# Kernel tuning notes

Measured on AMD Instinct MI355X. Metric: run time of the kernel, lower is better.

The kernel has to match this reference:

```python
import jax, jax.numpy as jnp
import numpy as np

B, S, H, F, E, G = 2, 2048, 1024, 2048, 16, 4
EPG = E // G            # experts per group
TOPK = 4                # experts_per_token == gate.top_k
TOPG = min(2, G)        # top groups considered


def setup_inputs() -> dict:
    key = jax.random.key(0)
    ks = jax.random.split(key, 8)
    def w(i, shape, fan):
        return jax.random.normal(ks[i], shape, jnp.float32) / np.sqrt(fan)
    pr = np.ones(E, np.float32)
    pr[::EPG] = 1.2  # expert_priority: first expert of each group boosted
    return dict(
        x=jax.random.normal(ks[0], (B, S, H), jnp.float32),
        Wg=w(1, (H, G), H), bg=jnp.zeros((G,), jnp.float32),
        Wr=w(2, (G, EPG, H), H), br=jnp.zeros((G, EPG), jnp.float32),
        Wc1=w(3, (H, H // 4), H), bc1=jnp.zeros((H // 4,), jnp.float32),
        Wc2=w(4, (H // 4, 1), H // 4), bc2=jnp.zeros((1,), jnp.float32),
        priority=jnp.asarray(pr),
        W1=w(5, (E, H, F), H), b1=jnp.zeros((E, F), jnp.float32),
        W2=w(6, (E, F, H), F), b2=jnp.zeros((E, H), jnp.float32),
    )


def _gate(xf, Wg, bg, Wr, br, Wc1, bc1, Wc2, bc2, priority):
    # xf: [N, H] flattened tokens. Eval mode: no router jitter.
    N = xf.shape[0]
    # confidence estimator: Linear -> GELU -> Linear -> Sigmoid  [N, 1]
    conf = jax.nn.sigmoid(jax.nn.gelu(xf @ Wc1 + bc1, approximate=False) @ Wc2 + bc2)
    group_probs = jax.nn.softmax(xf @ Wg + bg, axis=-1)              # [N, G]
    tg_p, tg_i = jax.lax.top_k(group_probs, TOPG)                    # [N, TOPG]
    # all group routers at once (G*EPG logits per token is tiny)
    logits = (jnp.einsum('nh,geh->nge', xf, Wr) + br) * priority.reshape(G, EPG)[None]
    probs = jax.nn.softmax(logits, axis=-1)                          # [N, G, EPG]
    c = conf[:, :, None]                                             # [N, 1, 1]
    probs = probs * c + (1.0 - c) / EPG                              # confidence blend
    scores = jnp.zeros((N, E), xf.dtype)
    rows = jnp.arange(N)[:, None]
    k_in = min(TOPK, EPG)
    for g in range(TOPG):  # top-group slots are disjoint -> collision-free set
        gid = tg_i[:, g]                                             # [N]
        pg = jnp.take_along_axis(probs, gid[:, None, None], axis=1)[:, 0, :]  # [N, EPG]
        tp, ti = jax.lax.top_k(pg, k_in)                             # [N, k_in]
        glob = ti + gid[:, None] * EPG                               # global expert ids
        scores = scores.at[rows, glob].set(tp * tg_p[:, g:g + 1])
    scores = scores / (scores.sum(-1, keepdims=True) + 1e-9)
    ts, ti2 = jax.lax.top_k(scores, TOPK)
    combine = jnp.zeros_like(scores).at[rows, ti2].set(ts)           # dispatch == combine
    return combine


def reference(x, Wg, bg, Wr, br, Wc1, bc1, Wc2, bc2, priority, W1, b1, W2, b2):
    b, s, h = x.shape
    xf = x.reshape(-1, h)                                            # [N, H]
    combine = _gate(xf, Wg, bg, Wr, br, Wc1, bc1, Wc2, bc2, priority)  # [N, E]
    # Torch loop applies every expert to every token, weighted by combine column.
    hid = jax.nn.gelu(jnp.einsum('nh,ehf->nef', xf, W1) + b1, approximate=False)  # [N,E,F]
    out_e = jnp.einsum('nef,efh->neh', hid, W2) + b2                 # [N, E, H]
    out = jnp.einsum('ne,neh->nh', combine, out_e)                   # [N, H]
    aux_loss = jnp.float32(0.0)  # eval mode
    return out.reshape(b, s, h), aux_loss
```

## Files before the change

### kernel.cpp

```cpp
#include <hip/hip_runtime.h>

#define H_DIM 1024
#define F_DIM 2048
#define NE 16
#define NG 4
#define EPG_C 4
#define NTOK 4096
#define NROWS 16384
#define HID_ROWS (NROWS + 128)
#define TB 8

using bf16x8 = __attribute__((ext_vector_type(8))) short;
using f32x4  = __attribute__((ext_vector_type(4))) float;

__device__ __forceinline__ float gelu_f(float v) {
    return 0.5f * v * (1.0f + erff(v * 0.70710678118654752440f));
}
__device__ __forceinline__ unsigned short f2bf(float f) {
    unsigned int u = __float_as_uint(f);
    u += 0x7FFFu + ((u >> 16) & 1u);
    return (unsigned short)(u >> 16);
}
__device__ __forceinline__ float bf2f(unsigned short s) {
    return __uint_as_float(((unsigned int)s) << 16);
}
__device__ __forceinline__ void split2(float v, unsigned short& hi, unsigned short& lo) {
    hi = f2bf(v);
    lo = f2bf(v - bf2f(hi));
}
__device__ __forceinline__ float wave_red_sum(float v) {
    #pragma unroll
    for (int off = 32; off > 0; off >>= 1) v += __shfl_down(v, off, 64);
    return v;
}
__device__ __forceinline__ void gld16(const void* g, void* l) {
    __builtin_amdgcn_global_load_lds(
        (const __attribute__((address_space(1))) unsigned int*)g,
        (__attribute__((address_space(3))) unsigned int*)l, 16, 0, 0);
}

__global__ __launch_bounds__(256) void zero_kernel(float* __restrict__ out, int n,
                                                   int* __restrict__ counts) {
    int i = blockIdx.x * blockDim.x + threadIdx.x;
    int stride = gridDim.x * blockDim.x;
    for (; i < n; i += stride) out[i] = 0.0f;
    if (blockIdx.x == 0 && threadIdx.x < NE) counts[threadIdx.x] = 0;
}

__global__ __launch_bounds__(256) void splitx_kernel(const float* __restrict__ x,
                                                     unsigned short* __restrict__ xh,
                                                     unsigned short* __restrict__ xl, int n4) {
    int i = blockIdx.x * blockDim.x + threadIdx.x;
    int stride = gridDim.x * blockDim.x;
    for (; i < n4; i += stride) {
        float4 v = ((const float4*)x)[i];
        ushort4 h, l;
        split2(v.x, h.x, l.x); split2(v.y, h.y, l.y);
        split2(v.z, h.z, l.z); split2(v.w, h.w, l.w);
        ((ushort4*)xh)[i] = h;
        ((ushort4*)xl)[i] = l;
    }
}

__global__ __launch_bounds__(256) void splitT_kernel(const float* __restrict__ W,
                                                     unsigned short* __restrict__ Th,
                                                     unsigned short* __restrict__ Tl,
                                                     int K, int N) {
    __shared__ float st[64][65];
    int e = blockIdx.z, kt = blockIdx.y, ntile = blockIdx.x;
    const float* src = W + (size_t)e * K * N + (size_t)kt * 64 * N + (size_t)ntile * 64;
    int t = threadIdx.x;
    int tr = t >> 4, tc = t & 15;
    #pragma unroll
    for (int i = 0; i < 4; ++i) {
        int row = tr + i * 16;
        float4 v = *(const float4*)(src + (size_t)row * N + tc * 4);
        st[row][tc * 4 + 0] = v.x; st[row][tc * 4 + 1] = v.y;
        st[row][tc * 4 + 2] = v.z; st[row][tc * 4 + 3] = v.w;
    }
    __syncthreads();
    unsigned short* dh = Th + (size_t)e * N * K + (size_t)ntile * 64 * K + kt * 64;
    unsigned short* dl = Tl + (size_t)e * N * K + (size_t)ntile * 64 * K + kt * 64;
    #pragma unroll
    for (int i = 0; i < 4; ++i) {
        int nl = tr + i * 16;
        ushort4 h4, l4;
        float v0 = st[tc * 4 + 0][nl], v1 = st[tc * 4 + 1][nl];
        float v2 = st[tc * 4 + 2][nl], v3 = st[tc * 4 + 3][nl];
        split2(v0, h4.x, l4.x); split2(v1, h4.y, l4.y);
        split2(v2, h4.z, l4.z); split2(v3, h4.w, l4.w);
        *(ushort4*)(dh + (size_t)nl * K + tc * 4) = h4;
        *(ushort4*)(dl + (size_t)nl * K + tc * 4) = l4;
    }
}

__global__ __launch_bounds__(256) void gate_kernel(
    const float* __restrict__ x, const float* __restrict__ Wg, const float* __restrict__ bg,
    const float* __restrict__ Wr, const float* __restrict__ br,
    const float* __restrict__ Wc1, const float* __restrict__ bc1,
    const float* __restrict__ Wc2, const float* __restrict__ bc2,
    const float* __restrict__ priority,
    int* __restrict__ counts, int* __restrict__ tok_list, float* __restrict__ wt_list)
{
    __shared__ float xs[TB][H_DIM];
    __shared__ float c1s[TB][256];
    __shared__ float lg_s[TB][20];
    __shared__ float conf_s[TB];

    const int tid = threadIdx.x;
    const int t0 = blockIdx.x * TB;

    {
        const float4* xv = (const float4*)(x + (size_t)t0 * H_DIM);
        float4* xsv = (float4*)&xs[0][0];
        #pragma unroll
        for (int i = 0; i < (TB * H_DIM / 4) / 256; ++i) xsv[tid + i * 256] = xv[tid + i * 256];
    }
    __syncthreads();

    {
        float acc[TB];
        #pragma unroll
        for (int t = 0; t < TB; ++t) acc[t] = 0.f;
        for (int k = 0; k < H_DIM; k += 4) {
            float w0 = Wc1[(k + 0) * 256 + tid];
            float w1 = Wc1[(k + 1) * 256 + tid];
            float w2 = Wc1[(k + 2) * 256 + tid];
            float w3 = Wc1[(k + 3) * 256 + tid];
            #pragma unroll
            for (int t = 0; t < TB; ++t) {
                float4 xv4 = *(const float4*)&xs[t][k];
                acc[t] += xv4.x * w0 + xv4.y * w1 + xv4.z * w2 + xv4.w * w3;
            }
        }
        float b = bc1[tid];
        #pragma unroll
        for (int t = 0; t < TB; ++t) c1s[t][tid] = gelu_f(acc[t] + b);
    }
    __syncthreads();

    const int wid = tid >> 6;
    const int lane = tid & 63;

    for (int t = wid; t < TB; t += 4) {
        float p = 0.f;
        #pragma unroll
        for (int j = 0; j < 4; ++j) {
            int idx = lane + 64 * j;
            p += c1s[t][idx] * Wc2[idx];
        }
        p = wave_red_sum(p);
        if (lane == 0) conf_s[t] = 1.0f / (1.0f + expf(-(p + bc2[0])));
    }

    for (int task = wid; task < TB * 20; task += 4) {
        int t = task / 20;
        int d = task % 20;
        float p = 0.f;
        if (d < NG) {
            #pragma unroll
            for (int j = 0; j < H_DIM / 64; ++j) {
                int k = lane + 64 * j;
                p += xs[t][k] * Wg[k * NG + d];
            }
        } else {
            const float* wr = Wr + (size_t)(d - NG) * H_DIM;
            #pragma unroll
            for (int j = 0; j < H_DIM / 64; ++j) {
                int k = lane + 64 * j;
                p += xs[t][k] * wr[k];
            }
        }
        p = wave_red_sum(p);
        if (lane == 0) lg_s[t][d] = p;
    }
    __syncthreads();

    if (tid < TB) {
        int t = tid;
        int token = t0 + t;
        float conf = conf_s[t];

        float gl[NG], gp[NG];
        float mg = -1e30f;
        #pragma unroll
        for (int i = 0; i < NG; ++i) { gl[i] = lg_s[t][i] + bg[i]; mg = fmaxf(mg, gl[i]); }
        float sg = 0.f;
        #pragma unroll
        for (int i = 0; i < NG; ++i) { gp[i] = expf(gl[i] - mg); sg += gp[i]; }
        #pragma unroll
        for (int i = 0; i < NG; ++i) gp[i] /= sg;

        int g0 = 0;
        for (int i = 1; i < NG; ++i) if (gp[i] > gp[g0]) g0 = i;
        int g1 = -1;
        for (int i = 0; i < NG; ++i) { if (i == g0) continue; if (g1 < 0 || gp[i] > gp[g1]) g1 = i; }

        float sc[NE];
        #pragma unroll
        for (int i = 0; i < NE; ++i) sc[i] = 0.f;
        int gids[2] = {g0, g1};
        float tgp[2] = {gp[g0], gp[g1]};
        for (int s = 0; s < 2; ++s) {
            int gg = gids[s];
            float l[EPG_C];
            float pm = -1e30f;
            #pragma unroll
            for (int e2 = 0; e2 < EPG_C; ++e2) {
                int ge = gg * EPG_C + e2;
                l[e2] = (lg_s[t][NG + ge] + br[ge]) * priority[ge];
                pm = fmaxf(pm, l[e2]);
            }
            float ps = 0.f;
            #pragma unroll
            for (int e2 = 0; e2 < EPG_C; ++e2) { l[e2] = expf(l[e2] - pm); ps += l[e2]; }
            #pragma unroll
            for (int e2 = 0; e2 < EPG_C; ++e2) {
                float p = l[e2] / ps;
                p = p * conf + (1.0f - conf) * 0.25f;
                sc[gg * EPG_C + e2] = p * tgp[s];
            }
        }
        float ssum = 0.f;
        #pragma unroll
        for (int i = 0; i < NE; ++i) ssum += sc[i];
        ssum += 1e-9f;
        #pragma unroll
        for (int i = 0; i < NE; ++i) sc[i] /= ssum;

        bool used[NE];
        #pragma unroll
        for (int i = 0; i < NE; ++i) used[i] = false;
        for (int kk = 0; kk < 4; ++kk) {
            int best = -1; float bv = -1e30f;
            for (int i = 0; i < NE; ++i) if (!used[i] && sc[i] > bv) { bv = sc[i]; best = i; }
            used[best] = true;
            int pos = atomicAdd(&counts[best], 1);
            tok_list[best * NTOK + pos] = token;
            wt_list[best * NTOK + pos] = bv;
        }
    }
}

__global__ void scan_kernel(const int* __restrict__ counts, int* __restrict__ offsets) {
    if (threadIdx.x == 0 && blockIdx.x == 0) {
        int s = 0;
        for (int e = 0; e < NE; ++e) { offsets[e] = s; s += counts[e]; }
    }
}

template<int KD, int ND, bool G1>
__global__ __launch_bounds__(256, 2) void gemm_mfma(
    const unsigned short* __restrict__ A_hi, const unsigned short* __restrict__ A_lo,
    const unsigned short* __restrict__ Bt_hi, const unsigned short* __restrict__ Bt_lo,
    const float* __restrict__ bias,
    const int* __restrict__ counts, const int* __restrict__ offsets,
    const int* __restrict__ tok_list, const float* __restrict__ wt_list,
    unsigned short* __restrict__ Chi, unsigned short* __restrict__ Clo,
    float* __restrict__ outp)
{
    constexpr int NT = ND / 128;
    const int MT = NTOK / 128;
    int bx = blockIdx.x;
    int e   = bx / (MT * NT);
    int rem = bx % (MT * NT);
    int mt = rem / NT, nt = rem % NT;
    int cnt = counts[e];
    if (mt * 128 >= cnt) return;
    int base = offsets[e];

    __shared__ unsigned short sm[4 * 128 * 64];
    unsigned short* smA_hi = sm;
    unsigned short* smA_lo = sm + 128 * 64;
    unsigned short* smB_hi = sm + 2 * 128 * 64;
    unsigned short* smB_lo = sm + 3 * 128 * 64;

    const int tid = threadIdx.x;
    const int lane = tid & 63;
    const int wid = tid >> 6;
    const int wr = wid >> 1, wc = wid & 1;
    const int l7 = lane & 7, l15 = lane & 15, lg = lane >> 4;
    const int srow = lane >> 3;
    const int schunk = (lane & 7) ^ srow;

    int ro_[4];
    size_t bo_[4];
    const size_t bbase = (size_t)e * ND * KD + (size_t)nt * 128 * KD;
    #pragma unroll
    for (int i = 0; i < 4; ++i) {
        int rloc = wid * 32 + i * 8 + srow;
        if (G1) {
            int r = min(mt * 128 + rloc, cnt - 1);
            ro_[i] = tok_list[e * NTOK + r] * KD;
        } else {
            ro_[i] = (base + mt * 128 + rloc) * KD;
        }
        bo_[i] = bbase + (size_t)rloc * KD;
    }

    f32x4 acc[4][4];
    #pragma unroll
    for (int m = 0; m < 4; ++m)
        #pragma unroll
        for (int n = 0; n < 4; ++n)
            #pragma unroll
            for (int j = 0; j < 4; ++j) acc[m][n][j] = 0.0f;

    for (int ks = 0; ks < KD / 64; ++ks) {
        __syncthreads();
        const int k0 = ks * 64;
        #pragma unroll
        for (int i = 0; i < 4; ++i) {
            const int R0 = wid * 32 + i * 8;
            gld16(A_hi + ro_[i] + k0 + schunk * 8, smA_hi + R0 * 64);
            gld16(A_lo + ro_[i] + k0 + schunk * 8, smA_lo + R0 * 64);
            gld16(Bt_hi + bo_[i] + k0 + schunk * 8, smB_hi + R0 * 64);
            gld16(Bt_lo + bo_[i] + k0 + schunk * 8, smB_lo + R0 * 64);
        }
        __syncthreads();

        #pragma unroll
        for (int kk = 0; kk < 2; ++kk) {
            bf16x8 ah[4], al[4], bh[4], bl[4];
            #pragma unroll
            for (int m = 0; m < 4; ++m) {
                int row = wr * 64 + m * 16 + l15;
                int eo = row * 64 + (((kk * 4 + lg) ^ l7) * 8);
                ah[m] = *(const bf16x8*)(smA_hi + eo);
                al[m] = *(const bf16x8*)(smA_lo + eo);
            }
            #pragma unroll
            for (int n = 0; n < 4; ++n) {
                int row = wc * 64 + n * 16 + l15;
                int eo = row * 64 + (((kk * 4 + lg) ^ l7) * 8);
                bh[n] = *(const bf16x8*)(smB_hi + eo);
                bl[n] = *(const bf16x8*)(smB_lo + eo);
            }
            #pragma unroll
            for (int m = 0; m < 4; ++m)
                #pragma unroll
                for (int n = 0; n < 4; ++n) {
                    acc[m][n] = __builtin_amdgcn_mfma_f32_16x16x32_bf16(ah[m], bh[n], acc[m][n], 0, 0, 0);
                    acc[m][n] = __builtin_amdgcn_mfma_f32_16x16x32_bf16(ah[m], bl[n], acc[m][n], 0, 0, 0);
                    acc[m][n] = __builtin_amdgcn_mfma_f32_16x16x32_bf16(al[m], bh[n], acc[m][n], 0, 0, 0);
                }
        }
    }

    #pragma unroll
    for (int m = 0; m < 4; ++m) {
        #pragma unroll
        for (int reg = 0; reg < 4; ++reg) {
            int row = mt * 128 + wr * 64 + m * 16 + lg * 4 + reg;
            if (row >= cnt) continue;
            if (G1) {
                #pragma unroll
                for (int n = 0; n < 4; ++n) {
                    int col = nt * 128 + wc * 64 + n * 16 + l15;
                    float v = gelu_f(acc[m][n][reg] + bias[e * ND + col]);
                    unsigned short hi, lo;
                    split2(v, hi, lo);
                    size_t o = (size_t)(base + row) * ND + col;
                    Chi[o] = hi;
                    Clo[o] = lo;
                }
            } else {
                int tok = tok_list[e * NTOK + row];
                float w = wt_list[e * NTOK + row];
                #pragma unroll
                for (int n = 0; n < 4; ++n) {
                    int col = nt * 128 + wc * 64 + n * 16 + l15;
                    float v = (acc[m][n][reg] + bias[e * ND + col]) * w;
                    atomicAdd(&outp[(size_t)tok * ND + col], v);
                }
            }
        }
    }
}

__global__ __launch_bounds__(256) void gemm1_f32(
    const float* __restrict__ x, const float* __restrict__ W1, const float* __restrict__ b1,
    const int* __restrict__ counts, const int* __restrict__ offsets,
    const int* __restrict__ tok_list, float* __restrict__ hid)
{
    const int NT = F_DIM / 64;
    const int MT = NTOK / 64;
    int bx = blockIdx.x;
    int e   = bx / (MT * NT);
    int rem = bx % (MT * NT);
    int mt = rem / NT;
    int nt = rem % NT;
    int cnt = counts[e];
    if (mt * 64 >= cnt) return;

    __shared__ float As[16][68];
    __shared__ float Bs[16][64];

    int tid = threadIdx.x;
    int aRow = tid >> 2, aSeg = tid & 3;
    int bRow = tid >> 4, bSeg = tid & 15;
    int ty = tid >> 4, tx = tid & 15;

    int gRow = mt * 64 + aRow;
    bool aValid = gRow < cnt;
    const float* aPtr = x;
    if (aValid) {
        int tok = tok_list[e * NTOK + gRow];
        aPtr = x + (size_t)tok * H_DIM + aSeg * 4;
    }
    const float* bPtr = W1 + (size_t)e * H_DIM * F_DIM + (size_t)bRow * F_DIM + nt * 64 + bSeg * 4;

    float acc[4][4];
    #pragma unroll
    for (int i = 0; i < 4; ++i)
        #pragma unroll
        for (int j = 0; j < 4; ++j) acc[i][j] = 0.f;

    for (int k0 = 0; k0 < H_DIM; k0 += 16) {
        float4 a4 = make_float4(0.f, 0.f, 0.f, 0.f);
        if (aValid) a4 = *(const float4*)(aPtr + k0);
        float4 b4 = *(const float4*)(bPtr + (size_t)k0 * F_DIM);
        __syncthreads();
        As[aSeg * 4 + 0][aRow] = a4.x;
        As[aSeg * 4 + 1][aRow] = a4.y;
        As[aSeg * 4 + 2][aRow] = a4.z;
        As[aSeg * 4 + 3][aRow] = a4.w;
        *(float4*)&Bs[bRow][bSeg * 4] = b4;
        __syncthreads();
        #pragma unroll
        for (int kk = 0; kk < 16; ++kk) {
            float4 av = *(const float4*)&As[kk][ty * 4];
            float4 bv = *(const float4*)&Bs[kk][tx * 4];
            float a[4] = {av.x, av.y, av.z, av.w};
            float b[4] = {bv.x, bv.y, bv.z, bv.w};
            #pragma unroll
            for (int i = 0; i < 4; ++i)
                #pragma unroll
                for (int j = 0; j < 4; ++j)
                    acc[i][j] = fmaf(a[i], b[j], acc[i][j]);
        }
    }

    int base = offsets[e];
    #pragma unroll
    for (int i = 0; i < 4; ++i) {
        int r = mt * 64 + ty * 4 + i;
        if (r >= cnt) continue;
        size_t rowOff = (size_t)(base + r) * F_DIM;
        #pragma unroll
        for (int j = 0; j < 4; ++j) {
            int c = nt * 64 + tx * 4 + j;
            hid[rowOff + c] = gelu_f(acc[i][j] + b1[e * F_DIM + c]);
        }
    }
}

__global__ __launch_bounds__(256) void gemm2_f32(
    const float* __restrict__ hid, const float* __restrict__ W2, const float* __restrict__ b2,
    const int* __restrict__ counts, const int* __restrict__ offsets,
    const int* __restrict__ tok_list, const float* __restrict__ wt_list,
    float* __restrict__ out)
{
    const int NT = H_DIM / 64;
    const int MT = NTOK / 64;
    int bx = blockIdx.x;
    int e   = bx / (MT * NT);
    int rem = bx % (MT * NT);
    int mt = rem / NT;
    int nt = rem % NT;
    int cnt = counts[e];
    if (mt * 64 >= cnt) return;
    int base = offsets[e];

    __shared__ float As[16][68];
    __shared__ float Bs[16][64];

    int tid = threadIdx.x;
    int aRow = tid >> 2, aSeg = tid & 3;
    int bRow = tid >> 4, bSeg = tid & 15;
    int ty = tid >> 4, tx = tid & 15;

    int gRow = mt * 64 + aRow;
    bool aValid = gRow < cnt;
    const float* aPtr = hid;
    if (aValid) aPtr = hid + (size_t)(base + gRow) * F_DIM + aSeg * 4;
    const float* bPtr = W2 + (size_t)e * F_DIM * H_DIM + (size_t)bRow * H_DIM + nt * 64 + bSeg * 4;

    float acc[4][4];
    #pragma unroll
    for (int i = 0; i < 4; ++i)
        #pragma unroll
        for (int j = 0; j < 4; ++j) acc[i][j] = 0.f;

    for (int k0 = 0; k0 < F_DIM; k0 += 16) {
        float4 a4 = make_float4(0.f, 0.f, 0.f, 0.f);
        if (aValid) a4 = *(const float4*)(aPtr + k0);
        float4 b4 = *(const float4*)(bPtr + (size_t)k0 * H_DIM);
        __syncthreads();
        As[aSeg * 4 + 0][aRow] = a4.x;
        As[aSeg * 4 + 1][aRow] = a4.y;
        As[aSeg * 4 + 2][aRow] = a4.z;
        As[aSeg * 4 + 3][aRow] = a4.w;
        *(float4*)&Bs[bRow][bSeg * 4] = b4;
        __syncthreads();
        #pragma unroll
        for (int kk = 0; kk < 16; ++kk) {
            float4 av = *(const float4*)&As[kk][ty * 4];
            float4 bv = *(const float4*)&Bs[kk][tx * 4];
            float a[4] = {av.x, av.y, av.z, av.w};
            float b[4] = {bv.x, bv.y, bv.z, bv.w};
            #pragma unroll
            for (int i = 0; i < 4; ++i)
                #pragma unroll
                for (int j = 0; j < 4; ++j)
                    acc[i][j] = fmaf(a[i], b[j], acc[i][j]);
        }
    }

    #pragma unroll
    for (int i = 0; i < 4; ++i) {
        int r = mt * 64 + ty * 4 + i;
        if (r >= cnt) continue;
        int tok  = tok_list[e * NTOK + r];
        float w  = wt_list[e * NTOK + r];
        #pragma unroll
        for (int j = 0; j < 4; ++j) {
            int c = nt * 64 + tx * 4 + j;
            atomicAdd(&out[(size_t)tok * H_DIM + c], (acc[i][j] + b2[e * H_DIM + c]) * w);
        }
    }
}

#define OFF_COUNTS  0
#define OFF_OFFSETS 256
#define OFF_TOK     512
#define OFF_WTL     (512 + NE * NTOK * 4)
#define OFF_XH      (1ull << 20)
#define OFF_XL      (OFF_XH + (size_t)NTOK * H_DIM * 2)
#define OFF_HIDH    (OFF_XL + (size_t)NTOK * H_DIM * 2)
#define OFF_HIDL    (OFF_HIDH + (size_t)HID_ROWS * F_DIM * 2)
#define OFF_WTH     (OFF_HIDL + (size_t)HID_ROWS * F_DIM * 2)
#define OFF_WTLO    (OFF_WTH + (size_t)NE * H_DIM * F_DIM * 2)
#define WS_NEED     (OFF_WTLO + (size_t)NE * H_DIM * F_DIM * 2)

extern "C" void kernel_launch(void* const* d_in, const int* in_sizes, int n_in,
                              void* d_out, int out_size, void* d_ws, size_t ws_size,
                              hipStream_t stream)
{
    const float* x   = (const float*)d_in[0];
    const float* Wg  = (const float*)d_in[1];
    const float* bg  = (const float*)d_in[2];
    const float* Wr  = (const float*)d_in[3];
    const float* br  = (const float*)d_in[4];
    const float* Wc1 = (const float*)d_in[5];
    const float* bc1 = (const float*)d_in[6];
    const float* Wc2 = (const float*)d_in[7];
    const float* bc2 = (const float*)d_in[8];
    const float* pri = (const float*)d_in[9];
    const float* W1  = (const float*)d_in[10];
    const float* b1  = (const float*)d_in[11];
    const float* W2  = (const float*)d_in[12];
    const float* b2  = (const float*)d_in[13];
    float* out = (float*)d_out;

    char* ws = (char*)d_ws;
    int*   counts   = (int*)(ws + OFF_COUNTS);
    int*   offsets  = (int*)(ws + OFF_OFFSETS);
    int*   tok_list = (int*)(ws + OFF_TOK);
    float* wt_list  = (float*)(ws + OFF_WTL);

    zero_kernel<<<2048, 256, 0, stream>>>(out, out_size, counts);
    gate_kernel<<<NTOK / TB, 256, 0, stream>>>(x, Wg, bg, Wr, br, Wc1, bc1, Wc2, bc2, pri,
                                               counts, tok_list, wt_list);
    scan_kernel<<<1, 64, 0, stream>>>(counts, offsets);

    if (ws_size >= WS_NEED) {
        unsigned short* xh   = (unsigned short*)(ws + OFF_XH);
        unsigned short* xl   = (unsigned short*)(ws + OFF_XL);
        unsigned short* hidh = (unsigned short*)(ws + OFF_HIDH);
        unsigned short* hidl = (unsigned short*)(ws + OFF_HIDL);
        unsigned short* wth  = (unsigned short*)(ws + OFF_WTH);
        unsigned short* wtl  = (unsigned short*)(ws + OFF_WTLO);

        splitx_kernel<<<2048, 256, 0, stream>>>(x, xh, xl, NTOK * H_DIM / 4);
        splitT_kernel<<<dim3(F_DIM / 64, H_DIM / 64, NE), 256, 0, stream>>>(W1, wth, wtl,
                                                                            H_DIM, F_DIM);
        gemm_mfma<H_DIM, F_DIM, true><<<NE * (NTOK / 128) * (F_DIM / 128), 256, 0, stream>>>(
            xh, xl, wth, wtl, b1, counts, offsets, tok_list, wt_list, hidh, hidl, nullptr);
        splitT_kernel<<<dim3(H_DIM / 64, F_DIM / 64, NE), 256, 0, stream>>>(W2, wth, wtl,
                                                                            F_DIM, H_DIM);
        gemm_mfma<F_DIM, H_DIM, false><<<NE * (NTOK / 128) * (H_DIM / 128), 256, 0, stream>>>(
            hidh, hidl, wth, wtl, b2, counts, offsets, tok_list, wt_list, nullptr, nullptr, out);
    } else {
        float* hid = (float*)(ws + (1 << 20));
        gemm1_f32<<<NE * (NTOK / 64) * (F_DIM / 64), 256, 0, stream>>>(x, W1, b1, counts, offsets,
                                                                       tok_list, hid);
        gemm2_f32<<<NE * (NTOK / 64) * (H_DIM / 64), 256, 0, stream>>>(hid, W2, b2, counts, offsets,
                                                                       tok_list, wt_list, out);
    }
}
```

Baseline: 1.112 ms.

## Double-buffer MFMA GEMM shared memory with 8-wave blocks and XCD-aware block remap

Rewrites the grouped expert GEMM to use 512-thread blocks (8 waves, each computing a 64x32 sub-tile) with a double-buffered 128 KB dynamic LDS, so the next K-slice's global-to-LDS loads are issued before the current slice's MFMAs. Each pair of waves now loads one of the four hi/lo operand arrays, which cuts per-thread address setup. It also remaps block IDs across the 8 XCDs so that neighbouring tiles share L2, and raises wave priority around the MFMA bursts. The trade-off is one block per CU because of the large LDS, which lowers occupancy, and tiles that early-exit when an expert has few tokens now idle a bigger block.

```diff
diff --git a/kernel.cpp b/kernel.cpp
--- a/kernel.cpp
+++ b/kernel.cpp
@@ -249,8 +249,10 @@
     }
 }
 
+#define ABUF (128 * 64)
+
 template<int KD, int ND, bool G1>
-__global__ __launch_bounds__(256, 2) void gemm_mfma(
+__global__ __launch_bounds__(512, 1) void gemm_mfma(
     const unsigned short* __restrict__ A_hi, const unsigned short* __restrict__ A_lo,
     const unsigned short* __restrict__ Bt_hi, const unsigned short* __restrict__ Bt_lo,
     const float* __restrict__ bias,
@@ -259,9 +261,15 @@
     unsigned short* __restrict__ Chi, unsigned short* __restrict__ Clo,
     float* __restrict__ outp)
 {
+    extern __shared__ unsigned short sm[];
+
     constexpr int NT = ND / 128;
     const int MT = NTOK / 128;
-    int bx = blockIdx.x;
+
+    int nwg = gridDim.x;
+    int bx0 = blockIdx.x;
+    int bx = (bx0 & 7) * (nwg >> 3) + (bx0 >> 3);
+
     int e   = bx / (MT * NT);
     int rem = bx % (MT * NT);
     int mt = rem / NT, nt = rem % NT;
@@ -269,59 +277,71 @@
     if (mt * 128 >= cnt) return;
     int base = offsets[e];
 
-    __shared__ unsigned short sm[4 * 128 * 64];
-    unsigned short* smA_hi = sm;
-    unsigned short* smA_lo = sm + 128 * 64;
-    unsigned short* smB_hi = sm + 2 * 128 * 64;
-    unsigned short* smB_lo = sm + 3 * 128 * 64;
-
     const int tid = threadIdx.x;
     const int lane = tid & 63;
     const int wid = tid >> 6;
-    const int wr = wid >> 1, wc = wid & 1;
+    const int wr = wid >> 2, wc = wid & 3;
     const int l7 = lane & 7, l15 = lane & 15, lg = lane >> 4;
+
+    const int arr  = wid >> 1;
+    const int half = wid & 1;
     const int srow = lane >> 3;
     const int schunk = (lane & 7) ^ srow;
 
-    int ro_[4];
-    size_t bo_[4];
+    const unsigned short* gsrc =
+        (arr == 0) ? A_hi : (arr == 1) ? A_lo : (arr == 2) ? Bt_hi : Bt_lo;
     const size_t bbase = (size_t)e * ND * KD + (size_t)nt * 128 * KD;
-    #pragma unroll
-    for (int i = 0; i < 4; ++i) {
-        int rloc = wid * 32 + i * 8 + srow;
-        if (G1) {
-            int r = min(mt * 128 + rloc, cnt - 1);
-            ro_[i] = tok_list[e * NTOK + r] * KD;
+
+    size_t roff[8];
+    #pragma unroll
+    for (int i = 0; i < 8; ++i) {
+        int rloc = half * 64 + i * 8 + srow;
+        if (arr < 2) {
+            if (G1) {
+                int r = min(mt * 128 + rloc, cnt - 1);
+                roff[i] = (size_t)tok_list[e * NTOK + r] * KD;
+            } else {
+                roff[i] = (size_t)(base + mt * 128 + rloc) * KD;
+            }
         } else {
-            ro_[i] = (base + mt * 128 + rloc) * KD;
-        }
-        bo_[i] = bbase + (size_t)rloc * KD;
-    }
-
-    f32x4 acc[4][4];
+            roff[i] = bbase + (size_t)rloc * KD;
+        }
+    }
+    unsigned short* ldst0 = sm + arr * ABUF + (half * 64) * 64;
+
+    f32x4 acc[4][2];
     #pragma unroll
     for (int m = 0; m < 4; ++m)
         #pragma unroll
-        for (int n = 0; n < 4; ++n)
+        for (int n = 0; n < 2; ++n)
             #pragma unroll
             for (int j = 0; j < 4; ++j) acc[m][n][j] = 0.0f;
 
-    for (int ks = 0; ks < KD / 64; ++ks) {
-        __syncthreads();
-        const int k0 = ks * 64;
-        #pragma unroll
-        for (int i = 0; i < 4; ++i) {
-            const int R0 = wid * 32 + i * 8;
-            gld16(A_hi + ro_[i] + k0 + schunk * 8, smA_hi + R0 * 64);
-            gld16(A_lo + ro_[i] + k0 + schunk * 8, smA_lo + R0 * 64);
-            gld16(Bt_hi + bo_[i] + k0 + schunk * 8, smB_hi + R0 * 64);
-            gld16(Bt_lo + bo_[i] + k0 + schunk * 8, smB_lo + R0 * 64);
-        }
-        __syncthreads();
+    constexpr int NK = KD / 64;
+
+    #pragma unroll
+    for (int i = 0; i < 8; ++i)
+        gld16(gsrc + roff[i] + schunk * 8, ldst0 + i * 8 * 64);
+    __syncthreads();
+
+    for (int ks = 0; ks < NK; ++ks) {
+        if (ks + 1 < NK) {
+            const int k0 = (ks + 1) * 64;
+            unsigned short* ld = ldst0 + ((ks + 1) & 1) * (4 * ABUF);
+            #pragma unroll
+            for (int i = 0; i < 8; ++i)
+                gld16(gsrc + roff[i] + k0 + schunk * 8, ld + i * 8 * 64);
+        }
+
+        const unsigned short* s0 = sm + (size_t)(ks & 1) * (4 * ABUF);
+        const unsigned short* smA_hi = s0;
+        const unsigned short* smA_lo = s0 + ABUF;
+        const unsigned short* smB_hi = s0 + 2 * ABUF;
+        const unsigned short* smB_lo = s0 + 3 * ABUF;
 
         #pragma unroll
         for (int kk = 0; kk < 2; ++kk) {
-            bf16x8 ah[4], al[4], bh[4], bl[4];
+            bf16x8 ah[4], al[4], bh[2], bl[2];
             #pragma unroll
             for (int m = 0; m < 4; ++m) {
                 int row = wr * 64 + m * 16 + l15;
@@ -330,21 +350,24 @@
                 al[m] = *(const bf16x8*)(smA_lo + eo);
             }
             #pragma unroll
-            for (int n = 0; n < 4; ++n) {
-                int row = wc * 64 + n * 16 + l15;
+            for (int n = 0; n < 2; ++n) {
+                int row = wc * 32 + n * 16 + l15;
                 int eo = row * 64 + (((kk * 4 + lg) ^ l7) * 8);
                 bh[n] = *(const bf16x8*)(smB_hi + eo);
                 bl[n] = *(const bf16x8*)(smB_lo + eo);
             }
+            __builtin_amdgcn_s_setprio(1);
             #pragma unroll
             for (int m = 0; m < 4; ++m)
                 #pragma unroll
-                for (int n = 0; n < 4; ++n) {
+                for (int n = 0; n < 2; ++n) {
                     acc[m][n] = __builtin_amdgcn_mfma_f32_16x16x32_bf16(ah[m], bh[n], acc[m][n], 0, 0, 0);
                     acc[m][n] = __builtin_amdgcn_mfma_f32_16x16x32_bf16(ah[m], bl[n], acc[m][n], 0, 0, 0);
                     acc[m][n] = __builtin_amdgcn_mfma_f32_16x16x32_bf16(al[m], bh[n], acc[m][n], 0, 0, 0);
                 }
-        }
+            __builtin_amdgcn_s_setprio(0);
+        }
+        __syncthreads();
     }
 
     #pragma unroll
@@ -355,8 +378,8 @@
             if (row >= cnt) continue;
             if (G1) {
                 #pragma unroll
-                for (int n = 0; n < 4; ++n) {
-                    int col = nt * 128 + wc * 64 + n * 16 + l15;
+                for (int n = 0; n < 2; ++n) {
+                    int col = nt * 128 + wc * 32 + n * 16 + l15;
                     float v = gelu_f(acc[m][n][reg] + bias[e * ND + col]);
                     unsigned short hi, lo;
                     split2(v, hi, lo);
@@ -368,8 +391,8 @@
                 int tok = tok_list[e * NTOK + row];
                 float w = wt_list[e * NTOK + row];
                 #pragma unroll
-                for (int n = 0; n < 4; ++n) {
-                    int col = nt * 128 + wc * 64 + n * 16 + l15;
+                for (int n = 0; n < 2; ++n) {
+                    int col = nt * 128 + wc * 32 + n * 16 + l15;
                     float v = (acc[m][n][reg] + bias[e * ND + col]) * w;
                     atomicAdd(&outp[(size_t)tok * ND + col], v);
                 }
@@ -582,14 +605,20 @@
         unsigned short* wth  = (unsigned short*)(ws + OFF_WTH);
         unsigned short* wtl  = (unsigned short*)(ws + OFF_WTLO);
 
+        const size_t shmem = 2 * 4 * (size_t)ABUF * sizeof(unsigned short);
+        (void)hipFuncSetAttribute((const void*)&gemm_mfma<H_DIM, F_DIM, true>,
+                                  hipFuncAttributeMaxDynamicSharedMemorySize, (int)shmem);
+        (void)hipFuncSetAttribute((const void*)&gemm_mfma<F_DIM, H_DIM, false>,
+                                  hipFuncAttributeMaxDynamicSharedMemorySize, (int)shmem);
+
         splitx_kernel<<<2048, 256, 0, stream>>>(x, xh, xl, NTOK * H_DIM / 4);
         splitT_kernel<<<dim3(F_DIM / 64, H_DIM / 64, NE), 256, 0, stream>>>(W1, wth, wtl,
                                                                             H_DIM, F_DIM);
-        gemm_mfma<H_DIM, F_DIM, true><<<NE * (NTOK / 128) * (F_DIM / 128), 256, 0, stream>>>(
+        gemm_mfma<H_DIM, F_DIM, true><<<NE * (NTOK / 128) * (F_DIM / 128), 512, shmem, stream>>>(
             xh, xl, wth, wtl, b1, counts, offsets, tok_list, wt_list, hidh, hidl, nullptr);
         splitT_kernel<<<dim3(H_DIM / 64, F_DIM / 64, NE), 256, 0, stream>>>(W2, wth, wtl,
                                                                             F_DIM, H_DIM);
-        gemm_mfma<F_DIM, H_DIM, false><<<NE * (NTOK / 128) * (H_DIM / 128), 256, 0, stream>>>(
+        gemm_mfma<F_DIM, H_DIM, false><<<NE * (NTOK / 128) * (H_DIM / 128), 512, shmem, stream>>>(
             hidh, hidl, wth, wtl, b2, counts, offsets, tok_list, wt_list, nullptr, nullptr, out);
     } else {
         float* hid = (float*)(ws + (1 << 20));
```

After: 1.132 ms. No clear change (+1.9%).
